# Performance work log

Hardware: AMD Instinct MI355X
Metric: run time of the kernel (lower is better)

Reference implementation:

```python
import jax, jax.numpy as jnp
import numpy as np

REG = 0.1      # ot_reg (entropic regularization)
TAU = 0.5      # ot_tau (marginal relaxation reg_m)
N_ITERS = 100  # fixed iteration count (POT default numItermax=1000 with early stop)


def setup_inputs() -> dict:
    key = jax.random.key(0)
    kx, ky = jax.random.split(key)
    x = jax.random.normal(kx, (8192, 1, 512), dtype=jnp.float32)
    y = jax.random.normal(ky, (4096, 1, 512), dtype=jnp.float32)
    return {"x": x, "y": y}


def _normalize_feature(x):
    # x - x.min(-1, keepdim)  (shift each row to be non-negative-min)
    return x - jnp.min(x, axis=-1, keepdims=True)


def reference(x, y):
    # x: (N,1,D), y: (M,1,D)
    x = _normalize_feature(x[:, 0, :])  # (N,D)
    y = _normalize_feature(y[:, 0, :])  # (M,D)

    # squared euclidean cost: cdist(x,y)**2, via gram trick (N,M)
    x2 = jnp.sum(x * x, axis=1)[:, None]
    y2 = jnp.sum(y * y, axis=1)[None, :]
    cost = jnp.maximum(x2 + y2 - 2.0 * (x @ y.T), 0.0)

    # normalized, detached cost used for the OT solve
    Mn = jax.lax.stop_gradient(cost / jnp.max(cost))
    K = jnp.exp(-Mn / REG)  # (N,M) Gibbs kernel

    n, m = K.shape
    a = 1.0 / n  # uniform source marginal (scalar since all entries equal)
    b = 1.0 / m  # uniform target marginal
    fi = TAU / (TAU + REG)

    u0 = jnp.full((n,), 1.0 / n, dtype=K.dtype)
    v0 = jnp.full((m,), 1.0 / m, dtype=K.dtype)

    def step(carry, _):
        u, v = carry
        u = (a / (K @ v)) ** fi       # (N,)
        v = (b / (K.T @ u)) ** fi     # (M,)
        return (u, v), None

    (u, v), _ = jax.lax.scan(step, (u0, v0), None, length=N_ITERS)

    flow = u[:, None] * K * v[None, :]          # (N,M), detached w.r.t. cost
    dist = jnp.sum(cost * flow)                  # scalar, grads flow via cost

    pi = flow.T[None, None, :, :]                # (1,1,M,N)
    return pi, dist
```

## Files before the change

### kernel.cpp

```cpp
#include <hip/hip_runtime.h>

#define N_ROWS 8192
#define M_ROWS 4096
#define D_DIM  512
#define N_ITERS 100
constexpr size_t NM = (size_t)N_ROWS * (size_t)M_ROWS;
constexpr float FREG   = 0.1f;
constexpr float FI     = 0.5f / (0.5f + 0.1f);
constexpr float A_MARG = 1.0f / (float)N_ROWS;
constexpr float B_MARG = 1.0f / (float)M_ROWS;

__device__ __forceinline__ unsigned short f2bf(float f) {
    unsigned int u = __float_as_uint(f);
    u += 0x7fffu + ((u >> 16) & 1u);
    return (unsigned short)(u >> 16);
}
__device__ __forceinline__ float bflo(unsigned int u) { return __uint_as_float(u << 16); }
__device__ __forceinline__ float bfhi(unsigned int u) { return __uint_as_float(u & 0xffff0000u); }
__device__ __forceinline__ unsigned int pack2(float a, float b) {
    return (unsigned int)f2bf(a) | ((unsigned int)f2bf(b) << 16);
}

__global__ void __launch_bounds__(256) init_kernel(float* v, unsigned int* maxc, float* dist) {
    int t = blockIdx.x * 256 + threadIdx.x;
    if (t < M_ROWS) v[t] = B_MARG;
    if (t == 0) { *maxc = 0u; *dist = 0.0f; }
}

__global__ void __launch_bounds__(256) rownorm_kernel(const float* __restrict__ x,
                                                      unsigned short* __restrict__ xn,
                                                      float* __restrict__ x2) {
    int lane = threadIdx.x & 63;
    int row  = blockIdx.x * 4 + (threadIdx.x >> 6);
    const float* p = x + (size_t)row * D_DIM + lane * 8;
    float4 v0 = *(const float4*)p;
    float4 v1 = *(const float4*)(p + 4);
    float a[8] = {v0.x, v0.y, v0.z, v0.w, v1.x, v1.y, v1.z, v1.w};
    float mn = a[0];
#pragma unroll
    for (int t = 1; t < 8; ++t) mn = fminf(mn, a[t]);
#pragma unroll
    for (int o = 32; o >= 1; o >>= 1) mn = fminf(mn, __shfl_xor(mn, o, 64));
    float ss = 0.0f;
#pragma unroll
    for (int t = 0; t < 8; ++t) { a[t] -= mn; ss = fmaf(a[t], a[t], ss); }
#pragma unroll
    for (int o = 32; o >= 1; o >>= 1) ss += __shfl_xor(ss, o, 64);
    uint4 pk;
    pk.x = pack2(a[0], a[1]); pk.y = pack2(a[2], a[3]);
    pk.z = pack2(a[4], a[5]); pk.w = pack2(a[6], a[7]);
    *(uint4*)(xn + (size_t)row * D_DIM + lane * 8) = pk;
    if (lane == 0) x2[row] = ss;
}

typedef __attribute__((ext_vector_type(8))) short short8;
typedef __attribute__((ext_vector_type(4))) float f32x4;

__global__ void __launch_bounds__(256) gemm_cost_kernel(const unsigned short* __restrict__ xn,
                                                        const unsigned short* __restrict__ yn,
                                                        const float* __restrict__ x2,
                                                        const float* __restrict__ y2,
                                                        unsigned short* __restrict__ cost,
                                                        unsigned int* __restrict__ maxc) {
    __shared__ unsigned short As[128 * 40];
    __shared__ unsigned short Bs[128 * 40];
    __shared__ float wred[4];
    int tid = threadIdx.x, lane = tid & 63, w = tid >> 6;
    int wm = w >> 1, wn = w & 1;
    int i0 = blockIdx.x * 128, j0 = blockIdx.y * 128;
    int lr = tid >> 2;
    int lq = tid & 3;
    f32x4 acc[4][4] = {};
    int m = lane & 15, quad = lane >> 4;

    for (int k0 = 0; k0 < D_DIM; k0 += 32) {
        uint4 a0 = *(const uint4*)(xn + (size_t)(i0 + lr) * D_DIM + k0 + lq * 8);
        uint4 a1 = *(const uint4*)(xn + (size_t)(i0 + lr + 64) * D_DIM + k0 + lq * 8);
        uint4 b0 = *(const uint4*)(yn + (size_t)(j0 + lr) * D_DIM + k0 + lq * 8);
        uint4 b1 = *(const uint4*)(yn + (size_t)(j0 + lr + 64) * D_DIM + k0 + lq * 8);
        __syncthreads();
        *(uint4*)&As[lr * 40 + lq * 8]        = a0;
        *(uint4*)&As[(lr + 64) * 40 + lq * 8] = a1;
        *(uint4*)&Bs[lr * 40 + lq * 8]        = b0;
        *(uint4*)&Bs[(lr + 64) * 40 + lq * 8] = b1;
        __syncthreads();
        short8 af[4], bfr[4];
#pragma unroll
        for (int t = 0; t < 4; ++t) {
            af[t]  = *(const short8*)&As[(wm * 64 + t * 16 + m) * 40 + quad * 8];
            bfr[t] = *(const short8*)&Bs[(wn * 64 + t * 16 + m) * 40 + quad * 8];
        }
#pragma unroll
        for (int tm = 0; tm < 4; ++tm)
#pragma unroll
            for (int tn = 0; tn < 4; ++tn)
                acc[tm][tn] = __builtin_amdgcn_mfma_f32_16x16x32_bf16(af[tm], bfr[tn], acc[tm][tn], 0, 0, 0);
    }

    float mymax = 0.0f;
#pragma unroll
    for (int tm = 0; tm < 4; ++tm) {
#pragma unroll
        for (int tn = 0; tn < 4; ++tn) {
            int col = j0 + wn * 64 + tn * 16 + m;
            float yv = y2[col];
#pragma unroll
            for (int t = 0; t < 4; ++t) {
                int row = i0 + wm * 64 + tm * 16 + quad * 4 + t;
                float c = fmaxf(x2[row] + yv - 2.0f * acc[tm][tn][t], 0.0f);
                mymax = fmaxf(mymax, c);
                cost[(size_t)row * M_ROWS + col] = f2bf(c);
            }
        }
    }
#pragma unroll
    for (int o = 32; o >= 1; o >>= 1) mymax = fmaxf(mymax, __shfl_xor(mymax, o, 64));
    if (lane == 0) wred[w] = mymax;
    __syncthreads();
    if (tid == 0) {
        float mx = fmaxf(fmaxf(wred[0], wred[1]), fmaxf(wred[2], wred[3]));
        atomicMax(maxc, __float_as_uint(mx));
    }
}

__global__ void __launch_bounds__(256) expT_kernel(unsigned short* __restrict__ Kmat,
                                                   unsigned short* __restrict__ KTmat,
                                                   const unsigned int* __restrict__ maxcb) {
    __shared__ unsigned int tl[64 * 33];
    float scale = -(1.0f / FREG) / __uint_as_float(*maxcb);
    int i0 = blockIdx.x * 64, j0 = blockIdx.y * 64;
    int tid = threadIdx.x;
    int b = tid & 7;
    int rp = tid >> 3;
    size_t base0 = (size_t)(i0 + 2 * rp) * M_ROWS + j0 + b * 8;
    uint4 c0 = *(const uint4*)(Kmat + base0);
    uint4 c1 = *(const uint4*)(Kmat + base0 + M_ROWS);
    unsigned int cc0[4] = {c0.x, c0.y, c0.z, c0.w};
    unsigned int cc1[4] = {c1.x, c1.y, c1.z, c1.w};
    float k0[8], k1[8];
#pragma unroll
    for (int t = 0; t < 4; ++t) {
        k0[2 * t]     = expf(bflo(cc0[t]) * scale);
        k0[2 * t + 1] = expf(bfhi(cc0[t]) * scale);
        k1[2 * t]     = expf(bflo(cc1[t]) * scale);
        k1[2 * t + 1] = expf(bfhi(cc1[t]) * scale);
    }
    uint4 o0, o1;
    o0.x = pack2(k0[0], k0[1]); o0.y = pack2(k0[2], k0[3]);
    o0.z = pack2(k0[4], k0[5]); o0.w = pack2(k0[6], k0[7]);
    o1.x = pack2(k1[0], k1[1]); o1.y = pack2(k1[2], k1[3]);
    o1.z = pack2(k1[4], k1[5]); o1.w = pack2(k1[6], k1[7]);
    *(uint4*)(Kmat + base0)          = o0;
    *(uint4*)(Kmat + base0 + M_ROWS) = o1;
#pragma unroll
    for (int t = 0; t < 8; ++t)
        tl[(b * 8 + t) * 33 + rp] = pack2(k0[t], k1[t]);
    __syncthreads();
    int c = tid >> 2, q = tid & 3;
    unsigned int o[8];
#pragma unroll
    for (int k = 0; k < 8; ++k) o[k] = tl[c * 33 + q * 8 + k];
    uint4 w0 = {o[0], o[1], o[2], o[3]};
    uint4 w1 = {o[4], o[5], o[6], o[7]};
    size_t ob = (size_t)(j0 + c) * N_ROWS + i0 + q * 16;
    *(uint4*)(KTmat + ob)     = w0;
    *(uint4*)(KTmat + ob + 8) = w1;
}

__global__ void __launch_bounds__(256) u_step_kernel(const unsigned short* __restrict__ Km,
                                                     const float* __restrict__ v,
                                                     float* __restrict__ u) {
    __shared__ __align__(16) float sv[M_ROWS];
    int tid = threadIdx.x, lane = tid & 63, w = tid >> 6;
    for (int i = tid; i < M_ROWS / 4; i += 256)
        ((float4*)sv)[i] = ((const float4*)v)[i];
    __syncthreads();
#pragma unroll
    for (int rr = 0; rr < 2; ++rr) {
        int r = blockIdx.x * 8 + w * 2 + rr;
        const unsigned short* kp = Km + (size_t)r * M_ROWS;
        float dot = 0.0f;
#pragma unroll
        for (int s = 0; s < 16; ++s) {
            int j = s * 256 + lane * 4;
            uint2 kk = *(const uint2*)(kp + j);
            float4 vv = *(const float4*)(sv + j);
            dot = fmaf(bflo(kk.x), vv.x, dot);
            dot = fmaf(bfhi(kk.x), vv.y, dot);
            dot = fmaf(bflo(kk.y), vv.z, dot);
            dot = fmaf(bfhi(kk.y), vv.w, dot);
        }
#pragma unroll
        for (int o = 32; o >= 1; o >>= 1) dot += __shfl_xor(dot, o, 64);
        if (lane == 0) u[r] = powf(A_MARG / dot, FI);
    }
}

__global__ void __launch_bounds__(256) v_step_kernel(const unsigned short* __restrict__ KTm,
                                                     const float* __restrict__ u,
                                                     float* __restrict__ v) {
    __shared__ __align__(16) float su[N_ROWS];
    int tid = threadIdx.x, lane = tid & 63, w = tid >> 6;
    for (int i = tid; i < N_ROWS / 4; i += 256)
        ((float4*)su)[i] = ((const float4*)u)[i];
    __syncthreads();
#pragma unroll
    for (int rr = 0; rr < 2; ++rr) {
        int r = blockIdx.x * 8 + w * 2 + rr;
        const unsigned short* kp = KTm + (size_t)r * N_ROWS;
        float dot = 0.0f;
#pragma unroll
        for (int s = 0; s < 32; ++s) {
            int j = s * 256 + lane * 4;
            uint2 kk = *(const uint2*)(kp + j);
            float4 vv = *(const float4*)(su + j);
            dot = fmaf(bflo(kk.x), vv.x, dot);
            dot = fmaf(bfhi(kk.x), vv.y, dot);
            dot = fmaf(bflo(kk.y), vv.z, dot);
            dot = fmaf(bfhi(kk.y), vv.w, dot);
        }
#pragma unroll
        for (int o = 32; o >= 1; o >>= 1) dot += __shfl_xor(dot, o, 64);
        if (lane == 0) v[r] = powf(B_MARG / dot, FI);
    }
}

__global__ void __launch_bounds__(256) finalize_kernel(const unsigned short* __restrict__ KTm,
                                                       const float* __restrict__ u,
                                                       const float* __restrict__ v,
                                                       const unsigned int* __restrict__ maxcb,
                                                       float* __restrict__ out,
                                                       float* __restrict__ dist) {
    __shared__ float red[4];
    int tid = threadIdx.x, lane = tid & 63;
    size_t base = ((size_t)blockIdx.x * 256 + tid) * 8;
    int mrow = (int)(base >> 13);
    int n    = (int)(base & 8191);
    float cscale = -FREG * __uint_as_float(*maxcb);
    uint4 kk = *(const uint4*)(KTm + base);
    float4 u0 = *(const float4*)(u + n);
    float4 u1 = *(const float4*)(u + n + 4);
    float vm = v[mrow];
    float kv[8] = {bflo(kk.x), bfhi(kk.x), bflo(kk.y), bfhi(kk.y),
                   bflo(kk.z), bfhi(kk.z), bflo(kk.w), bfhi(kk.w)};
    float uu[8] = {u0.x, u0.y, u0.z, u0.w, u1.x, u1.y, u1.z, u1.w};
    float fl[8];
    float ds = 0.0f;
#pragma unroll
    for (int t = 0; t < 8; ++t) {
        fl[t] = uu[t] * kv[t] * vm;
        ds = fmaf(cscale * logf(kv[t]), fl[t], ds);
    }
    float4 w0 = {fl[0], fl[1], fl[2], fl[3]};
    float4 w1 = {fl[4], fl[5], fl[6], fl[7]};
    *(float4*)(out + base)     = w0;
    *(float4*)(out + base + 4) = w1;
#pragma unroll
    for (int o = 32; o >= 1; o >>= 1) ds += __shfl_xor(ds, o, 64);
    if (lane == 0) red[tid >> 6] = ds;
    __syncthreads();
    if (tid == 0) atomicAdd(dist, red[0] + red[1] + red[2] + red[3]);
}

extern "C" void kernel_launch(void* const* d_in, const int* in_sizes, int n_in,
                              void* d_out, int out_size, void* d_ws, size_t ws_size,
                              hipStream_t stream) {
    const float* x = (const float*)d_in[0];
    const float* y = (const float*)d_in[1];
    float* out = (float*)d_out;
    char* ws = (char*)d_ws;

    unsigned short* Kmat = (unsigned short*)(ws);
    unsigned short* KT   = (unsigned short*)(ws + 67108864);
    unsigned short* xn   = (unsigned short*)(ws + 134217728);
    unsigned short* yn   = (unsigned short*)(ws + 142606336);
    float* x2            = (float*)(ws + 146800640);
    float* y2            = (float*)(ws + 146833408);
    float* u             = (float*)(ws + 146849792);
    float* v             = (float*)(ws + 146882560);
    unsigned int* maxc   = (unsigned int*)(ws + 146898944);
    float* dist = out + NM;

    init_kernel<<<16, 256, 0, stream>>>(v, maxc, dist);
    rownorm_kernel<<<N_ROWS / 4, 256, 0, stream>>>(x, xn, x2);
    rownorm_kernel<<<M_ROWS / 4, 256, 0, stream>>>(y, yn, y2);
    gemm_cost_kernel<<<dim3(N_ROWS / 128, M_ROWS / 128), 256, 0, stream>>>(xn, yn, x2, y2, Kmat, maxc);
    expT_kernel<<<dim3(N_ROWS / 64, M_ROWS / 64), 256, 0, stream>>>(Kmat, KT, maxc);

    for (int it = 0; it < N_ITERS; ++it) {
        u_step_kernel<<<N_ROWS / 8, 256, 0, stream>>>(Kmat, v, u);
        v_step_kernel<<<M_ROWS / 8, 256, 0, stream>>>(KT, u, v);
    }

    finalize_kernel<<<(unsigned)(NM / (8 * 256)), 256, 0, stream>>>(KT, u, v, maxc, out, dist);
}
```

Measured before the change: 3.038 ms.

## Drop LDS staging in Sinkhorn matvecs and replace atomic dist with two-pass reduction

The u/v matvec kernels no longer copy the whole v/u vector into shared memory per block. They read it straight from global/L2 with 16-byte loads, one row per wave, using four independent accumulators. This removes the per-block LDS fill and barrier and doubles the block count. The finalize kernel also writes per-block partial sums to a scratch buffer, and a single-block kernel then reduces them, replacing 16384 float atomics on one address with a deterministic reduction.

After: 2.750 ms. 9.5% less time.

```diff
diff --git a/kernel.cpp b/kernel.cpp
--- a/kernel.cpp
+++ b/kernel.cpp
@@ -9,6 +9,7 @@
 constexpr float FI     = 0.5f / (0.5f + 0.1f);
 constexpr float A_MARG = 1.0f / (float)N_ROWS;
 constexpr float B_MARG = 1.0f / (float)M_ROWS;
+#define FIN_BLOCKS 16384
 
 __device__ __forceinline__ unsigned short f2bf(float f) {
     unsigned int u = __float_as_uint(f);
@@ -21,10 +22,10 @@
     return (unsigned int)f2bf(a) | ((unsigned int)f2bf(b) << 16);
 }
 
-__global__ void __launch_bounds__(256) init_kernel(float* v, unsigned int* maxc, float* dist) {
+__global__ void __launch_bounds__(256) init_kernel(float* v, unsigned int* maxc) {
     int t = blockIdx.x * 256 + threadIdx.x;
     if (t < M_ROWS) v[t] = B_MARG;
-    if (t == 0) { *maxc = 0u; *dist = 0.0f; }
+    if (t == 0) *maxc = 0u;
 }
 
 __global__ void __launch_bounds__(256) rownorm_kernel(const float* __restrict__ x,
@@ -170,59 +171,57 @@
 __global__ void __launch_bounds__(256) u_step_kernel(const unsigned short* __restrict__ Km,
                                                      const float* __restrict__ v,
                                                      float* __restrict__ u) {
-    __shared__ __align__(16) float sv[M_ROWS];
     int tid = threadIdx.x, lane = tid & 63, w = tid >> 6;
-    for (int i = tid; i < M_ROWS / 4; i += 256)
-        ((float4*)sv)[i] = ((const float4*)v)[i];
-    __syncthreads();
-#pragma unroll
-    for (int rr = 0; rr < 2; ++rr) {
-        int r = blockIdx.x * 8 + w * 2 + rr;
-        const unsigned short* kp = Km + (size_t)r * M_ROWS;
-        float dot = 0.0f;
-#pragma unroll
-        for (int s = 0; s < 16; ++s) {
-            int j = s * 256 + lane * 4;
-            uint2 kk = *(const uint2*)(kp + j);
-            float4 vv = *(const float4*)(sv + j);
-            dot = fmaf(bflo(kk.x), vv.x, dot);
-            dot = fmaf(bfhi(kk.x), vv.y, dot);
-            dot = fmaf(bflo(kk.y), vv.z, dot);
-            dot = fmaf(bfhi(kk.y), vv.w, dot);
-        }
-#pragma unroll
-        for (int o = 32; o >= 1; o >>= 1) dot += __shfl_xor(dot, o, 64);
-        if (lane == 0) u[r] = powf(A_MARG / dot, FI);
-    }
+    int r = blockIdx.x * 4 + w;
+    const unsigned short* kp = Km + (size_t)r * M_ROWS + lane * 8;
+    const float* vp = v + lane * 8;
+    float a0 = 0.0f, a1 = 0.0f, a2 = 0.0f, a3 = 0.0f;
+#pragma unroll
+    for (int s = 0; s < 8; ++s) {
+        uint4 kk = *(const uint4*)(kp + s * 512);
+        float4 v0 = *(const float4*)(vp + s * 512);
+        float4 v1 = *(const float4*)(vp + s * 512 + 4);
+        a0 = fmaf(bflo(kk.x), v0.x, a0);
+        a1 = fmaf(bfhi(kk.x), v0.y, a1);
+        a2 = fmaf(bflo(kk.y), v0.z, a2);
+        a3 = fmaf(bfhi(kk.y), v0.w, a3);
+        a0 = fmaf(bflo(kk.z), v1.x, a0);
+        a1 = fmaf(bfhi(kk.z), v1.y, a1);
+        a2 = fmaf(bflo(kk.w), v1.z, a2);
+        a3 = fmaf(bfhi(kk.w), v1.w, a3);
+    }
+    float dot = (a0 + a1) + (a2 + a3);
+#pragma unroll
+    for (int o = 32; o >= 1; o >>= 1) dot += __shfl_xor(dot, o, 64);
+    if (lane == 0) u[r] = powf(A_MARG / dot, FI);
 }
 
 __global__ void __launch_bounds__(256) v_step_kernel(const unsigned short* __restrict__ KTm,
                                                      const float* __restrict__ u,
                                                      float* __restrict__ v) {
-    __shared__ __align__(16) float su[N_ROWS];
     int tid = threadIdx.x, lane = tid & 63, w = tid >> 6;
-    for (int i = tid; i < N_ROWS / 4; i += 256)
-        ((float4*)su)[i] = ((const float4*)u)[i];
-    __syncthreads();
-#pragma unroll
-    for (int rr = 0; rr < 2; ++rr) {
-        int r = blockIdx.x * 8 + w * 2 + rr;
-        const unsigned short* kp = KTm + (size_t)r * N_ROWS;
-        float dot = 0.0f;
-#pragma unroll
-        for (int s = 0; s < 32; ++s) {
-            int j = s * 256 + lane * 4;
-            uint2 kk = *(const uint2*)(kp + j);
-            float4 vv = *(const float4*)(su + j);
-            dot = fmaf(bflo(kk.x), vv.x, dot);
-            dot = fmaf(bfhi(kk.x), vv.y, dot);
-            dot = fmaf(bflo(kk.y), vv.z, dot);
-            dot = fmaf(bfhi(kk.y), vv.w, dot);
-        }
-#pragma unroll
-        for (int o = 32; o >= 1; o >>= 1) dot += __shfl_xor(dot, o, 64);
-        if (lane == 0) v[r] = powf(B_MARG / dot, FI);
-    }
+    int r = blockIdx.x * 4 + w;
+    const unsigned short* kp = KTm + (size_t)r * N_ROWS + lane * 8;
+    const float* up = u + lane * 8;
+    float a0 = 0.0f, a1 = 0.0f, a2 = 0.0f, a3 = 0.0f;
+#pragma unroll
+    for (int s = 0; s < 16; ++s) {
+        uint4 kk = *(const uint4*)(kp + s * 512);
+        float4 v0 = *(const float4*)(up + s * 512);
+        float4 v1 = *(const float4*)(up + s * 512 + 4);
+        a0 = fmaf(bflo(kk.x), v0.x, a0);
+        a1 = fmaf(bfhi(kk.x), v0.y, a1);
+        a2 = fmaf(bflo(kk.y), v0.z, a2);
+        a3 = fmaf(bfhi(kk.y), v0.w, a3);
+        a0 = fmaf(bflo(kk.z), v1.x, a0);
+        a1 = fmaf(bfhi(kk.z), v1.y, a1);
+        a2 = fmaf(bflo(kk.w), v1.z, a2);
+        a3 = fmaf(bfhi(kk.w), v1.w, a3);
+    }
+    float dot = (a0 + a1) + (a2 + a3);
+#pragma unroll
+    for (int o = 32; o >= 1; o >>= 1) dot += __shfl_xor(dot, o, 64);
+    if (lane == 0) v[r] = powf(B_MARG / dot, FI);
 }
 
 __global__ void __launch_bounds__(256) finalize_kernel(const unsigned short* __restrict__ KTm,
@@ -230,7 +229,7 @@
                                                        const float* __restrict__ v,
                                                        const unsigned int* __restrict__ maxcb,
                                                        float* __restrict__ out,
-                                                       float* __restrict__ dist) {
+                                                       float* __restrict__ part) {
     __shared__ float red[4];
     int tid = threadIdx.x, lane = tid & 63;
     size_t base = ((size_t)blockIdx.x * 256 + tid) * 8;
@@ -259,7 +258,20 @@
     for (int o = 32; o >= 1; o >>= 1) ds += __shfl_xor(ds, o, 64);
     if (lane == 0) red[tid >> 6] = ds;
     __syncthreads();
-    if (tid == 0) atomicAdd(dist, red[0] + red[1] + red[2] + red[3]);
+    if (tid == 0) part[blockIdx.x] = red[0] + red[1] + red[2] + red[3];
+}
+
+__global__ void __launch_bounds__(256) reduce_dist_kernel(const float* __restrict__ part,
+                                                          float* __restrict__ dist) {
+    __shared__ float red[4];
+    int tid = threadIdx.x, lane = tid & 63;
+    float s = 0.0f;
+    for (int i = tid; i < FIN_BLOCKS; i += 256) s += part[i];
+#pragma unroll
+    for (int o = 32; o >= 1; o >>= 1) s += __shfl_xor(s, o, 64);
+    if (lane == 0) red[tid >> 6] = s;
+    __syncthreads();
+    if (tid == 0) *dist = red[0] + red[1] + red[2] + red[3];
 }
 
 extern "C" void kernel_launch(void* const* d_in, const int* in_sizes, int n_in,
@@ -279,18 +291,20 @@
     float* u             = (float*)(ws + 146849792);
     float* v             = (float*)(ws + 146882560);
     unsigned int* maxc   = (unsigned int*)(ws + 146898944);
+    float* part          = (float*)(ws + 134217728);
     float* dist = out + NM;
 
-    init_kernel<<<16, 256, 0, stream>>>(v, maxc, dist);
+    init_kernel<<<16, 256, 0, stream>>>(v, maxc);
     rownorm_kernel<<<N_ROWS / 4, 256, 0, stream>>>(x, xn, x2);
     rownorm_kernel<<<M_ROWS / 4, 256, 0, stream>>>(y, yn, y2);
     gemm_cost_kernel<<<dim3(N_ROWS / 128, M_ROWS / 128), 256, 0, stream>>>(xn, yn, x2, y2, Kmat, maxc);
     expT_kernel<<<dim3(N_ROWS / 64, M_ROWS / 64), 256, 0, stream>>>(Kmat, KT, maxc);
 
     for (int it = 0; it < N_ITERS; ++it) {
-        u_step_kernel<<<N_ROWS / 8, 256, 0, stream>>>(Kmat, v, u);
-        v_step_kernel<<<M_ROWS / 8, 256, 0, stream>>>(KT, u, v);
-    }
-
-    finalize_kernel<<<(unsigned)(NM / (8 * 256)), 256, 0, stream>>>(KT, u, v, maxc, out, dist);
-}
+        u_step_kernel<<<N_ROWS / 4, 256, 0, stream>>>(Kmat, v, u);
+        v_step_kernel<<<M_ROWS / 4, 256, 0, stream>>>(KT, u, v);
+    }
+
+    finalize_kernel<<<FIN_BLOCKS, 256, 0, stream>>>(KT, u, v, maxc, out, part);
+    reduce_dist_kernel<<<1, 256, 0, stream>>>(part, dist);
+}
```
